# Kernel tuning notes

Hardware: AMD Instinct MI355X
Metric: run time of the kernel (lower is better)

Reference implementation:

```python
import jax, jax.numpy as jnp
import numpy as np

EPS = 1e-8  # `eps` is an undefined global in the original repo snippet; standard capsule eps
CH_J, N_J, R_NUM = 32, 4, 3


def _squash(s):
    # Faithful to the source: norm / (1 + norm^2 + eps) * s, norm over last dim (size 1 here)
    norm = jnp.sqrt(jnp.sum(s * s, axis=-1, keepdims=True))
    return norm / (1.0 + norm ** 2 + EPS) * s


def _unif_act_wt_entropy(k):
    # k: (b, W, W, 1, ch_j, ch_i); softmax was taken over (W, W, ch_j) per (b, ch_i).
    # Entropy of coupling coefficients normalized by uniform entropy, averaged.
    b, ci = k.shape[0], k.shape[-1]
    p = jnp.transpose(k, (0, 5, 3, 1, 2, 4)).reshape(b, ci, -1)
    ent = -jnp.sum(p * jnp.log(p + EPS), axis=-1)
    return jnp.mean(ent / jnp.log(jnp.asarray(p.shape[-1], p.dtype)))


def reference(inputs, conv_w, conv_b):
    b, ch_i, n_i, h, w = inputs.shape
    # (b, 1, ch_i*n_i, h, w) -> Conv3d stride (n_i,1,1), pad (0,1,1)
    x = inputs.reshape(b, 1, ch_i * n_i, h, w)
    x = jax.lax.conv_general_dilated(
        x, conv_w, window_strides=(n_i, 1, 1),
        padding=((0, 0), (1, 1), (1, 1)),
        dimension_numbers=('NCDHW', 'OIDHW', 'NCDHW'))
    x = x + conv_b[None, :, None, None, None]
    W = x.shape[-1]
    # (b, ch_i, ch_j*n_j, W, W) -> (b, W, W, n_j, ch_j, ch_i)
    x = jnp.transpose(x, (0, 2, 1, 3, 4)).reshape(b, ch_i, CH_J, N_J, W, W)
    x = jnp.transpose(x, (0, 4, 5, 3, 2, 1))

    B = jnp.zeros((b, W, W, 1, CH_J, ch_i), dtype=x.dtype)
    S_hat = None
    k = None
    for i in range(R_NUM):
        # softmax over (W, W, ch_j) jointly, per (b, ch_i)
        logits = jnp.transpose(B, (0, 5, 3, 1, 2, 4)).reshape(b, ch_i, 1, -1)
        k = jax.nn.softmax(logits, axis=-1)
        k = jnp.transpose(k.reshape(b, ch_i, 1, W, W, CH_J), (0, 3, 4, 2, 5, 1))
        S = jnp.sum(k * x, axis=-1, keepdims=True)  # (b, W, W, n_j, ch_j, 1)
        S_hat = _squash(S)
        if i < R_NUM - 1:
            B = B + jnp.sum(S_hat * x, axis=3, keepdims=True)

    out = jnp.transpose(S_hat[..., 0], (0, 4, 3, 1, 2))  # (b, ch_j, n_j, W, W)
    return out, _unif_act_wt_entropy(k)


def setup_inputs() -> dict:
    key = jax.random.key(0)
    k1, k2, k3 = jax.random.split(key, 3)
    inputs = jax.random.normal(k1, (8, 32, 8, 32, 32), dtype=jnp.float32)
    conv_w = jax.random.normal(k2, (128, 1, 3, 3, 3), dtype=jnp.float32) * 0.05
    conv_b = jax.random.normal(k3, (128,), dtype=jnp.float32) * 0.05
    return {"inputs": inputs, "conv_w": conv_w, "conv_b": conv_b}
```

## Files before the change

kernel.cpp:

```cpp
#include <hip/hip_runtime.h>
#include <hip/hip_bf16.h>

#define EPSF 1e-8f

typedef short bf16x8 __attribute__((ext_vector_type(8)));
typedef float f32x4 __attribute__((ext_vector_type(4)));


__device__ __forceinline__ float bflo(unsigned u){ return __uint_as_float(u<<16); }
__device__ __forceinline__ float bfhi(unsigned u){ return __uint_as_float(u&0xffff0000u); }
__device__ __forceinline__ float bfu16(unsigned short u){ return __uint_as_float((unsigned)u<<16); }
__device__ __forceinline__ unsigned bfpack2(float a,float b){
    return (__float_as_uint(a)>>16)|(__float_as_uint(b)&0xffff0000u);
}
__device__ __forceinline__ unsigned short bfr16(float a){
    return (unsigned short)(__float_as_uint(a)>>16);
}
__device__ __forceinline__ float fastrcp(float x){ return __builtin_amdgcn_rcpf(x); }
__device__ __forceinline__ bf16x8 pack8(const float* v){
    union { unsigned u[4]; bf16x8 v8; } cv;
#pragma unroll
    for (int j = 0; j < 4; ++j) cv.u[j] = bfpack2(v[2*j], v[2*j+1]);
    return cv.v8;
}

template<int PHASE>
__global__ __launch_bounds__(256, 4) void k_caps(
    const float* __restrict__ in, const float* __restrict__ cw,
    const float* __restrict__ cb, unsigned* __restrict__ Bpk,
    const float* __restrict__ sm_in, const float* __restrict__ siz_in,
    float* __restrict__ pm, float* __restrict__ ps, float* __restrict__ pt,
    float* __restrict__ shat) {
    __shared__ __align__(16) unsigned char smem[36480];
    float* slab = (float*)smem;
    unsigned short* wLT = (unsigned short*)(smem + 13824);
    float* cbL  = (float*)(smem + 21248);
    float* smL  = (float*)(smem + 21760);
    float* sizL = (float*)(smem + 21888);
    unsigned* ktab = (unsigned*)(smem + 22016);

    const int t = threadIdx.x;
    const int lane = t & 63, wid = t >> 6;
    const int bid = blockIdx.x;
    const int bh = bid >> 3, b = bh >> 5, h = bh & 31;
    const int w0 = (bid & 7) << 2;
    const int l15 = lane & 15, lq = lane >> 4;

    unsigned char* wb = smem + 22144 + (size_t)wid * 3584;
    unsigned* Bu  = (unsigned*)wb;
    float* shL    = (float*)(wb + 2560);
    float* auxL   = (float*)(wb + 3072);
    float* statb  = (float*)(wb + 3200);

    for (int j = t; j < 864; j += 256) {
        const int r = j / 3, q = j - r * 3;
        const int ci2 = r / 9, rem = r - ci2 * 9, kd = rem / 3, dy = rem - kd * 3;
        const int y = h + dy - 1;
        const int x0 = w0 - 4 + q * 4;
        float4 f = {0.f, 0.f, 0.f, 0.f};
        if ((unsigned)y < 32u && (unsigned)x0 < 32u)
            f = *reinterpret_cast<const float4*>(
                in + (((size_t)(b * 32 + ci2) * 8 + kd) * 32 + y) * 32 + x0);
        *reinterpret_cast<float4*>(slab + r * 12 + q * 4) = f;
    }
    for (int j = t; j < 3456; j += 256) {
        const int c = j / 27, k = j - c * 27;
        wLT[k * 132 + c] = bfr16(cw[j]);
    }
    if (t < 128) cbL[t] = cb[t];
    if (t < 32) {
        const int k = t < 27 ? t : 26;
        const int kd = k / 9, r9 = k - kd * 9, dy = r9 / 3, dx = r9 - dy * 3;
        ktab[t] = (unsigned)((kd * 3 + dy) * 12 + dx);
    }
    if constexpr (PHASE >= 1) {
        if (t < 32) { smL[t] = sm_in[b * 32 + t]; sizL[t] = siz_in[b * 32 + t]; }
    }
    __syncthreads();

    const size_t loc = (size_t)bh * 32 + w0 + wid;
    const int tb = wid + 3;

    float b1v[16];
    if constexpr (PHASE == 0) {
        const int k2 = lane >> 1, half = lane & 1;
        float vs = 0.f;
        if (k2 < 27) {
            const float* sp = slab + half * 16 * 108 + ktab[k2] + tb;
#pragma unroll
            for (int i = 0; i < 16; ++i) vs += sp[i * 108];
        }
        vs += __shfl_xor(vs, 1);
        if (half == 0 && k2 < 27) auxL[k2] = vs;
    } else {
        const uint4* Bg = (const uint4*)(Bpk + loc * 512 + (size_t)lane * 8);
        const uint4 q0 = Bg[0], q1 = Bg[1];
        const unsigned pk[8] = {q0.x, q0.y, q0.z, q0.w, q1.x, q1.y, q1.z, q1.w};
#pragma unroll
        for (int e = 0; e < 8; ++e) { b1v[2*e] = bflo(pk[e]); b1v[2*e+1] = bfhi(pk[e]); }
#pragma unroll
        for (int mt = 0; mt < 2; ++mt)
#pragma unroll
        for (int reg = 0; reg < 4; ++reg)
#pragma unroll
        for (int nt = 0; nt < 2; ++nt) {
            const float me = b1v[mt*8 + nt*4 + reg];
            const float ot = __shfl_xor(me, 1);
            const unsigned pku = (l15 & 1) ? bfpack2(ot, me) : bfpack2(me, ot);
            if ((l15 & 1) == nt)
                Bu[(mt*16 + lq*4 + reg)*20 + nt*8 + (l15 >> 1)] = pku;
        }
        bf16x8 kmA[2];
#pragma unroll
        for (int mt = 0; mt < 2; ++mt) {
            const uint4 q = *(const uint4*)(Bu + (mt*16 + l15)*20 + lq*4);
            const unsigned uu[4] = {q.x, q.y, q.z, q.w};
            float ev[8];
#pragma unroll
            for (int j2 = 0; j2 < 4; ++j2) {
                const int ci0 = lq*8 + 2*j2;
                ev[2*j2]   = __expf(bflo(uu[j2]) - smL[ci0])   * sizL[ci0];
                ev[2*j2+1] = __expf(bfhi(uu[j2]) - smL[ci0+1]) * sizL[ci0+1];
            }
            kmA[mt] = pack8(ev);
        }
        bf16x8 vtB[2];
#pragma unroll
        for (int nt = 0; nt < 2; ++nt) {
            const int kt = nt*16 + l15;
            const unsigned ko = ktab[kt];
            float vals[8];
#pragma unroll
            for (int j = 0; j < 8; ++j) {
                const float sv = slab[(lq*8 + j)*108 + ko + tb];
                vals[j] = (kt < 27) ? sv : (kt == 27 ? 1.0f : 0.0f);
            }
            vtB[nt] = pack8(vals);
        }
        f32x4 accu[2][2];
#pragma unroll
        for (int mt = 0; mt < 2; ++mt)
#pragma unroll
        for (int nt = 0; nt < 2; ++nt)
            accu[mt][nt] = __builtin_amdgcn_mfma_f32_16x16x32_bf16(
                kmA[mt], vtB[nt], (f32x4){0.f,0.f,0.f,0.f}, 0, 0, 0);
#pragma unroll
        for (int mt = 0; mt < 2; ++mt)
#pragma unroll
        for (int reg = 0; reg < 4; ++reg)
#pragma unroll
        for (int nt = 0; nt < 2; ++nt) {
            const float me = accu[mt][nt][reg];
            const float ot = __shfl_xor(me, 1);
            const unsigned pku = (l15 & 1) ? bfpack2(ot, me) : bfpack2(me, ot);
            if ((l15 & 1) == nt)
                Bu[(mt*16 + lq*4 + reg)*20 + nt*8 + (l15 >> 1)] = pku;
        }
    }

#pragma unroll
    for (int cc = 0; cc < 2; ++cc) {
        const int c = lane + cc * 64;
        float S;
        if constexpr (PHASE == 0) {
            S = 0.f;
#pragma unroll
            for (int k = 0; k < 27; ++k)
                S = fmaf(bfu16(wLT[k*132 + c]), auxL[k], S);
            S = S * (1.0f/32768.0f) + cbL[c] * (1.0f/1024.0f);
        } else {
            const unsigned* up = Bu + (c >> 2) * 20;
            S = 0.f;
#pragma unroll
            for (int p = 0; p < 13; ++p) {
                const unsigned u = up[p];
                S = fmaf(bfu16(wLT[(2*p)*132 + c]),   bflo(u), S);
                S = fmaf(bfu16(wLT[(2*p+1)*132 + c]), bfhi(u), S);
            }
            const unsigned u13 = up[13];
            S = fmaf(bfu16(wLT[26*132 + c]), bflo(u13), S);
            S = fmaf(cbL[c], bfhi(u13), S);
        }
        const float sq = fabsf(S) * S * fastrcp(1.f + S*S + EPSF);
        if constexpr (PHASE == 2) shat[loc * 128 + c] = sq;
        else shL[c] = sq;
    }
    if constexpr (PHASE == 2) return;

    {
        const int k0 = 2*l15, k1 = k0 + 1;
#pragma unroll
        for (int i = 0; i < 8; ++i) {
            const int cj = lq + 4*i;
            float v0 = 0.f, v1 = 0.f;
            if (k0 < 27) {
#pragma unroll
                for (int nj = 0; nj < 4; ++nj)
                    v0 = fmaf(shL[cj*4+nj], bfu16(wLT[k0*132 + cj*4 + nj]), v0);
            }
            if (k1 < 27) {
#pragma unroll
                for (int nj = 0; nj < 4; ++nj)
                    v1 = fmaf(shL[cj*4+nj], bfu16(wLT[k1*132 + cj*4 + nj]), v1);
            }
            Bu[cj*20 + l15] = bfpack2(v0, v1);
        }
        if (lane < 32) {
            float cv = 0.f;
#pragma unroll
            for (int nj = 0; nj < 4; ++nj)
                cv = fmaf(shL[lane*4+nj], cbL[lane*4+nj], cv);
            auxL[lane] = cv;
        }
    }

    bf16x8 wsA[2], vB[2];
#pragma unroll
    for (int mt = 0; mt < 2; ++mt) {
        union { uint4 q4; bf16x8 v8; } cv;
        cv.q4 = *(const uint4*)(Bu + (mt*16 + l15)*20 + lq*4);
        wsA[mt] = cv.v8;
    }
#pragma unroll
    for (int nt = 0; nt < 2; ++nt) {
        const int ci = nt*16 + l15;
        float vals[8];
#pragma unroll
        for (int j = 0; j < 8; ++j) {
            const int k = lq*8 + j;
            const float sv = slab[ci*108 + ktab[k] + tb];
            vals[j] = (k < 27) ? sv : 0.0f;
        }
        vB[nt] = pack8(vals);
    }
    f32x4 accb[2][2];
#pragma unroll
    for (int mt = 0; mt < 2; ++mt)
#pragma unroll
    for (int nt = 0; nt < 2; ++nt)
        accb[mt][nt] = __builtin_amdgcn_mfma_f32_16x16x32_bf16(
            wsA[mt], vB[nt], (f32x4){0.f,0.f,0.f,0.f}, 0, 0, 0);

    float bnew[16];
#pragma unroll
    for (int mt = 0; mt < 2; ++mt)
#pragma unroll
    for (int nt = 0; nt < 2; ++nt)
#pragma unroll
    for (int reg = 0; reg < 4; ++reg) {
        float val = accb[mt][nt][reg] + auxL[mt*16 + lq*4 + reg];
        if constexpr (PHASE == 1) val += b1v[mt*8 + nt*4 + reg];
        bnew[mt*8 + nt*4 + reg] = val;
    }
    {
        unsigned pk[8];
#pragma unroll
        for (int e = 0; e < 8; ++e) pk[e] = bfpack2(bnew[2*e], bnew[2*e+1]);
        uint4* Bg = (uint4*)(Bpk + loc * 512 + (size_t)lane * 8);
        Bg[0] = make_uint4(pk[0], pk[1], pk[2], pk[3]);
        Bg[1] = make_uint4(pk[4], pk[5], pk[6], pk[7]);
    }
    float m2[2], s2[2], T2[2];
#pragma unroll
    for (int nt = 0; nt < 2; ++nt) {
        float m = -1e30f;
#pragma unroll
        for (int mt = 0; mt < 2; ++mt)
#pragma unroll
        for (int reg = 0; reg < 4; ++reg) m = fmaxf(m, bnew[mt*8 + nt*4 + reg]);
        float s = 0.f, T = 0.f;
#pragma unroll
        for (int mt = 0; mt < 2; ++mt)
#pragma unroll
        for (int reg = 0; reg < 4; ++reg) {
            const float d = bnew[mt*8 + nt*4 + reg] - m;
            const float e = __expf(d);
            s += e; T += e * d;
        }
        m2[nt] = m; s2[nt] = s; T2[nt] = T;
#pragma unroll
        for (int off = 16; off <= 32; off <<= 1) {
            const float mo = __shfl_xor(m2[nt], off);
            const float so = __shfl_xor(s2[nt], off);
            const float To = __shfl_xor(T2[nt], off);
            const float nm = fmaxf(m2[nt], mo);
            const float ea = __expf(m2[nt]-nm), eb = __expf(mo-nm);
            T2[nt] = ea*(T2[nt] + s2[nt]*(m2[nt]-nm)) + eb*(To + so*(mo-nm));
            s2[nt] = ea*s2[nt] + eb*so;
            m2[nt] = nm;
        }
    }
    if (lane < 16) {
#pragma unroll
        for (int nt = 0; nt < 2; ++nt) {
            const int ci = nt*16 + lane;
            statb[ci] = m2[nt]; statb[32+ci] = s2[nt]; statb[64+ci] = T2[nt];
        }
    }
    __syncthreads();
    if (t < 32) {
        float M = -1e30f, Z = 0.f, T = 0.f;
#pragma unroll
        for (int wv = 0; wv < 4; ++wv) {
            const float* sw = (const float*)(smem + 22144 + wv*3584 + 3200);
            const float mo = sw[t], so = sw[32+t], To = sw[64+t];
            const float nm = fmaxf(M, mo);
            const float ea = __expf(M-nm), eb = __expf(mo-nm);
            T = ea*(T + Z*(M-nm)) + eb*(To + so*(mo-nm));
            Z = ea*Z + eb*so;
            M = nm;
        }
        pm[bid*32 + t] = M;
        ps[bid*32 + t] = Z;
        if constexpr (PHASE == 1) pt[bid*32 + t] = T;
    }
}

template <int NPART, bool ENT>
__global__ __launch_bounds__(256) void k_comb(const float* __restrict__ pm,
                                              const float* __restrict__ ps,
                                              const float* __restrict__ pt,
                                              float* __restrict__ sm,
                                              float* __restrict__ siz,
                                              float* __restrict__ entp) {
    const int b = blockIdx.x, t = threadIdx.x;
    const int ci = t & 31, seg = t >> 5;
    constexpr int PER = NPART / 8;
    __shared__ float red[3][8][33];

    float M = -1e30f;
    for (int k = 0; k < PER; ++k)
        M = fmaxf(M, pm[((size_t)b * NPART + seg * PER + k) * 32 + ci]);
    red[0][seg][ci] = M;
    __syncthreads();
    float Mg = red[0][0][ci];
#pragma unroll
    for (int q = 1; q < 8; ++q) Mg = fmaxf(Mg, red[0][q][ci]);

    float Z = 0.0f, T = 0.0f;
    for (int k = 0; k < PER; ++k) {
        const size_t i = ((size_t)b * NPART + seg * PER + k) * 32 + ci;
        const float dm = pm[i] - Mg;
        const float e = __expf(dm);
        Z += ps[i] * e;
        if constexpr (ENT) T += (pt[i] + ps[i] * dm) * e;
    }
    red[1][seg][ci] = Z;
    if constexpr (ENT) red[2][seg][ci] = T;
    __syncthreads();
    if (t < 32) {
        float Zt = 0.0f, Tt = 0.0f;
#pragma unroll
        for (int q = 0; q < 8; ++q) {
            Zt += red[1][q][ci];
            if constexpr (ENT) Tt += red[2][q][ci];
        }
        sm[b * 32 + ci] = Mg;
        siz[b * 32 + ci] = 1.0f / Zt;
        if constexpr (ENT)
            entp[b * 32 + ci] = (logf(Zt) - Tt / Zt) * (1.0f / 10.39720770839918f);
    }
}

__global__ __launch_bounds__(256) void k_out(const float* __restrict__ shat,
                                             const float* __restrict__ entp,
                                             float* __restrict__ out) {
    __shared__ float tile[32][129];
    const int bh = blockIdx.x;
    const int b = bh >> 5, h = bh & 31;
    const int t = threadIdx.x;
    const float4* sp = reinterpret_cast<const float4*>(shat + (size_t)bh * 4096);
#pragma unroll
    for (int j = 0; j < 4; ++j) {
        const int idx = t + j * 256;
        const float4 f = sp[idx];
        const int w = idx >> 5;
        const int c4 = (idx & 31) * 4;
        tile[w][c4 + 0] = f.x; tile[w][c4 + 1] = f.y;
        tile[w][c4 + 2] = f.z; tile[w][c4 + 3] = f.w;
    }
    __syncthreads();
    const int c = t >> 1, half = t & 1;
    float* op = out + (((size_t)b * 128 + c) * 32 + h) * 32 + half * 16;
#pragma unroll
    for (int j = 0; j < 16; ++j) op[j] = tile[half * 16 + j][c];

    if (bh == 0) {
        __shared__ float er[256];
        er[t] = entp[t];
        __syncthreads();
        for (int s2 = 128; s2 > 0; s2 >>= 1) {
            if (t < s2) er[t] += er[t + s2];
            __syncthreads();
        }
        if (t == 0) out[1048576] = er[0] * (1.0f / 256.0f);
    }
}

extern "C" void kernel_launch(void* const* d_in, const int* in_sizes, int n_in,
                              void* d_out, int out_size, void* d_ws, size_t ws_size,
                              hipStream_t stream) {
    const float* in = (const float*)d_in[0];
    const float* cw = (const float*)d_in[1];
    const float* cb = (const float*)d_in[2];
    float* out = (float*)d_out;

    unsigned* Bpk = (unsigned*)d_ws;
    float* shat = (float*)(Bpk + 4194304);
    float* pm0  = shat + 1048576;
    float* ps0  = pm0 + 65536;
    float* pm1  = ps0 + 65536;
    float* ps1  = pm1 + 65536;
    float* pt1  = ps1 + 65536;
    float* sm0  = pt1 + 65536;
    float* siz0 = sm0 + 256;
    float* sm1  = siz0 + 256;
    float* siz1 = sm1 + 256;
    float* entp = siz1 + 256;

    k_caps<0><<<2048, 256, 0, stream>>>(in, cw, cb, Bpk, sm0, siz0, pm0, ps0, pt1, shat);
    k_comb<256, false><<<8, 256, 0, stream>>>(pm0, ps0, nullptr, sm0, siz0, nullptr);
    k_caps<1><<<2048, 256, 0, stream>>>(in, cw, cb, Bpk, sm0, siz0, pm1, ps1, pt1, shat);
    k_comb<256, true><<<8, 256, 0, stream>>>(pm1, ps1, pt1, sm1, siz1, entp);
    k_caps<2><<<2048, 256, 0, stream>>>(in, cw, cb, Bpk, sm1, siz1, pm1, ps1, pt1, shat);
    k_out<<<256, 256, 0, stream>>>(shat, entp, out);
}
```

Before: 89.54 us.

## Store input slab as bf16 in LDS and fuse output transpose into final phase

```diff
diff --git a/kernel.cpp b/kernel.cpp
--- a/kernel.cpp
+++ b/kernel.cpp
@@ -25,19 +25,19 @@
 }
 
 template<int PHASE>
-__global__ __launch_bounds__(256, 4) void k_caps(
+__global__ __launch_bounds__(256, 5) void k_caps(
     const float* __restrict__ in, const float* __restrict__ cw,
     const float* __restrict__ cb, unsigned* __restrict__ Bpk,
     const float* __restrict__ sm_in, const float* __restrict__ siz_in,
     float* __restrict__ pm, float* __restrict__ ps, float* __restrict__ pt,
-    float* __restrict__ shat) {
-    __shared__ __align__(16) unsigned char smem[36480];
-    float* slab = (float*)smem;
-    unsigned short* wLT = (unsigned short*)(smem + 13824);
-    float* cbL  = (float*)(smem + 21248);
-    float* smL  = (float*)(smem + 21760);
-    float* sizL = (float*)(smem + 21888);
-    unsigned* ktab = (unsigned*)(smem + 22016);
+    float* __restrict__ outp) {
+    __shared__ __align__(16) unsigned char smem[29568];
+    unsigned short* slabB = (unsigned short*)smem;
+    unsigned short* wLT = (unsigned short*)(smem + 6912);
+    float* cbL  = (float*)(smem + 14336);
+    float* smL  = (float*)(smem + 14848);
+    float* sizL = (float*)(smem + 14976);
+    unsigned* ktab = (unsigned*)(smem + 15104);
 
     const int t = threadIdx.x;
     const int lane = t & 63, wid = t >> 6;
@@ -46,7 +46,7 @@
     const int w0 = (bid & 7) << 2;
     const int l15 = lane & 15, lq = lane >> 4;
 
-    unsigned char* wb = smem + 22144 + (size_t)wid * 3584;
+    unsigned char* wb = smem + 15232 + (size_t)wid * 3584;
     unsigned* Bu  = (unsigned*)wb;
     float* shL    = (float*)(wb + 2560);
     float* auxL   = (float*)(wb + 3072);
@@ -61,7 +61,9 @@
         if ((unsigned)y < 32u && (unsigned)x0 < 32u)
             f = *reinterpret_cast<const float4*>(
                 in + (((size_t)(b * 32 + ci2) * 8 + kd) * 32 + y) * 32 + x0);
-        *reinterpret_cast<float4*>(slab + r * 12 + q * 4) = f;
+        unsigned* sp = (unsigned*)slabB + r * 6 + q * 2;
+        sp[0] = bfpack2(f.x, f.y);
+        sp[1] = bfpack2(f.z, f.w);
     }
     for (int j = t; j < 3456; j += 256) {
         const int c = j / 27, k = j - c * 27;
@@ -86,9 +88,9 @@
         const int k2 = lane >> 1, half = lane & 1;
         float vs = 0.f;
         if (k2 < 27) {
-            const float* sp = slab + half * 16 * 108 + ktab[k2] + tb;
-#pragma unroll
-            for (int i = 0; i < 16; ++i) vs += sp[i * 108];
+            const unsigned short* sp = slabB + half * 16 * 108 + ktab[k2] + tb;
+#pragma unroll
+            for (int i = 0; i < 16; ++i) vs += bfu16(sp[i * 108]);
         }
         vs += __shfl_xor(vs, 1);
         if (half == 0 && k2 < 27) auxL[k2] = vs;
@@ -129,13 +131,13 @@
         for (int nt = 0; nt < 2; ++nt) {
             const int kt = nt*16 + l15;
             const unsigned ko = ktab[kt];
-            float vals[8];
+            union { unsigned short s[8]; bf16x8 v8; } cv;
 #pragma unroll
             for (int j = 0; j < 8; ++j) {
-                const float sv = slab[(lq*8 + j)*108 + ko + tb];
-                vals[j] = (kt < 27) ? sv : (kt == 27 ? 1.0f : 0.0f);
-            }
-            vtB[nt] = pack8(vals);
+                const unsigned short sv = slabB[(lq*8 + j)*108 + ko + tb];
+                cv.s[j] = (kt < 27) ? sv : (unsigned short)(kt == 27 ? 0x3f80 : 0);
+            }
+            vtB[nt] = cv.v8;
         }
         f32x4 accu[2][2];
 #pragma unroll
@@ -182,10 +184,32 @@
             S = fmaf(cbL[c], bfhi(u13), S);
         }
         const float sq = fabsf(S) * S * fastrcp(1.f + S*S + EPSF);
-        if constexpr (PHASE == 2) shat[loc * 128 + c] = sq;
-        else shL[c] = sq;
-    }
-    if constexpr (PHASE == 2) return;
+        shL[c] = sq;
+    }
+
+    if constexpr (PHASE == 2) {
+        __syncthreads();
+        if (t < 128) {
+            const float* s0 = (const float*)(smem + 15232 + 0*3584 + 2560);
+            const float* s1 = (const float*)(smem + 15232 + 1*3584 + 2560);
+            const float* s2 = (const float*)(smem + 15232 + 2*3584 + 2560);
+            const float* s3 = (const float*)(smem + 15232 + 3*3584 + 2560);
+            float4 o = make_float4(s0[t], s1[t], s2[t], s3[t]);
+            *reinterpret_cast<float4*>(
+                outp + ((size_t)(b*128 + t))*1024 + (size_t)h*32 + w0) = o;
+        }
+        if (bid == 0) {
+            float* er = (float*)smem;
+            er[t] = pt[t];
+            __syncthreads();
+            for (int s2v = 128; s2v > 0; s2v >>= 1) {
+                if (t < s2v) er[t] += er[t + s2v];
+                __syncthreads();
+            }
+            if (t == 0) outp[1048576] = er[0] * (1.0f/256.0f);
+        }
+        return;
+    }
 
     {
         const int k0 = 2*l15, k1 = k0 + 1;
@@ -224,14 +248,14 @@
 #pragma unroll
     for (int nt = 0; nt < 2; ++nt) {
         const int ci = nt*16 + l15;
-        float vals[8];
+        union { unsigned short s[8]; bf16x8 v8; } cv;
 #pragma unroll
         for (int j = 0; j < 8; ++j) {
             const int k = lq*8 + j;
-            const float sv = slab[ci*108 + ktab[k] + tb];
-            vals[j] = (k < 27) ? sv : 0.0f;
-        }
-        vB[nt] = pack8(vals);
+            const unsigned short sv = slabB[ci*108 + ktab[k] + tb];
+            cv.s[j] = (k < 27) ? sv : (unsigned short)0;
+        }
+        vB[nt] = cv.v8;
     }
     f32x4 accb[2][2];
 #pragma unroll
@@ -302,7 +326,7 @@
         float M = -1e30f, Z = 0.f, T = 0.f;
 #pragma unroll
         for (int wv = 0; wv < 4; ++wv) {
-            const float* sw = (const float*)(smem + 22144 + wv*3584 + 3200);
+            const float* sw = (const float*)(smem + 15232 + wv*3584 + 3200);
             const float mo = sw[t], so = sw[32+t], To = sw[64+t];
             const float nm = fmaxf(M, mo);
             const float ea = __expf(M-nm), eb = __expf(mo-nm);
@@ -362,41 +386,6 @@
     }
 }
 
-__global__ __launch_bounds__(256) void k_out(const float* __restrict__ shat,
-                                             const float* __restrict__ entp,
-                                             float* __restrict__ out) {
-    __shared__ float tile[32][129];
-    const int bh = blockIdx.x;
-    const int b = bh >> 5, h = bh & 31;
-    const int t = threadIdx.x;
-    const float4* sp = reinterpret_cast<const float4*>(shat + (size_t)bh * 4096);
-#pragma unroll
-    for (int j = 0; j < 4; ++j) {
-        const int idx = t + j * 256;
-        const float4 f = sp[idx];
-        const int w = idx >> 5;
-        const int c4 = (idx & 31) * 4;
-        tile[w][c4 + 0] = f.x; tile[w][c4 + 1] = f.y;
-        tile[w][c4 + 2] = f.z; tile[w][c4 + 3] = f.w;
-    }
-    __syncthreads();
-    const int c = t >> 1, half = t & 1;
-    float* op = out + (((size_t)b * 128 + c) * 32 + h) * 32 + half * 16;
-#pragma unroll
-    for (int j = 0; j < 16; ++j) op[j] = tile[half * 16 + j][c];
-
-    if (bh == 0) {
-        __shared__ float er[256];
-        er[t] = entp[t];
-        __syncthreads();
-        for (int s2 = 128; s2 > 0; s2 >>= 1) {
-            if (t < s2) er[t] += er[t + s2];
-            __syncthreads();
-        }
-        if (t == 0) out[1048576] = er[0] * (1.0f / 256.0f);
-    }
-}
-
 extern "C" void kernel_launch(void* const* d_in, const int* in_sizes, int n_in,
                               void* d_out, int out_size, void* d_ws, size_t ws_size,
                               hipStream_t stream) {
@@ -406,8 +395,7 @@
     float* out = (float*)d_out;
 
     unsigned* Bpk = (unsigned*)d_ws;
-    float* shat = (float*)(Bpk + 4194304);
-    float* pm0  = shat + 1048576;
+    float* pm0  = (float*)(Bpk + 4194304);
     float* ps0  = pm0 + 65536;
     float* pm1  = ps0 + 65536;
     float* ps1  = pm1 + 65536;
@@ -418,10 +406,9 @@
     float* siz1 = sm1 + 256;
     float* entp = siz1 + 256;
 
-    k_caps<0><<<2048, 256, 0, stream>>>(in, cw, cb, Bpk, sm0, siz0, pm0, ps0, pt1, shat);
+    k_caps<0><<<2048, 256, 0, stream>>>(in, cw, cb, Bpk, sm0, siz0, pm0, ps0, pt1, out);
     k_comb<256, false><<<8, 256, 0, stream>>>(pm0, ps0, nullptr, sm0, siz0, nullptr);
-    k_caps<1><<<2048, 256, 0, stream>>>(in, cw, cb, Bpk, sm0, siz0, pm1, ps1, pt1, shat);
+    k_caps<1><<<2048, 256, 0, stream>>>(in, cw, cb, Bpk, sm0, siz0, pm1, ps1, pt1, out);
     k_comb<256, true><<<8, 256, 0, stream>>>(pm1, ps1, pt1, sm1, siz1, entp);
-    k_caps<2><<<2048, 256, 0, stream>>>(in, cw, cb, Bpk, sm1, siz1, pm1, ps1, pt1, shat);
-    k_out<<<256, 256, 0, stream>>>(shat, entp, out);
-}
+    k_caps<2><<<2048, 256, 0, stream>>>(in, cw, cb, Bpk, sm1, siz1, pm1, ps1, entp, out);
+}
```

After: 85.61 us. 1.05x faster.
